# Optimization experiments

Hardware: AMD Instinct MI355X
Metric: run time of the kernel (lower is better)

Reference implementation:

```python
import jax, jax.numpy as jnp
import numpy as np

B, N, DIM = 2, 2048, 256
H, DH, M, NN, FF = 4, 64, 16, 32, 4
POS_DIM = 2 * FF + 1           # 9
EIN = DH                       # edge_input_dim (edge_dim = 0)
STD = 1e-3                     # init_eps


def setup_inputs() -> dict:
    key = jax.random.key(0)
    ks = jax.random.split(key, 16)
    w = lambda k, s: (jax.random.normal(k, s, jnp.float32) * STD)
    z = lambda s: jnp.zeros(s, jnp.float32)
    return {
        'feats': jax.random.normal(ks[0], (B, N, DIM), jnp.float32),
        'coors': jax.random.normal(ks[1], (B, N, 3), jnp.float32),
        'w_qkv': w(ks[2], (DIM, 3 * H * DH)),
        'w_out': w(ks[3], (H * DH, DIM)), 'b_out': z((DIM,)),
        'w_p1': w(ks[4], (POS_DIM, 2 * DH)), 'b_p1': z((2 * DH,)),
        'w_p2': w(ks[5], (2 * DH, DH)), 'b_p2': z((DH,)),
        'w_e1': w(ks[6], (EIN, 2 * EIN)), 'b_e1': z((2 * EIN,)),
        'w_e2': w(ks[7], (2 * EIN, M)), 'b_e2': z((M,)),
        'w_a1': w(ks[8], (M, 4 * M)), 'b_a1': z((4 * M,)),
        'w_a2': w(ks[9], (4 * M, 1)), 'b_a2': z((1,)),
        'w_c1': w(ks[10], (M * H, 4 * M)), 'b_c1': z((4 * M,)),
        'w_c2': w(ks[11], (4 * M, 1)), 'b_c2': z((1,)),
    }


def _forward(feats, coors, w_qkv, w_out, b_out, w_p1, b_p1, w_p2, b_p2,
             w_e1, b_e1, w_e2, b_e2, w_a1, b_a1, w_a2, b_a2,
             w_c1, b_c1, w_c2, b_c2):
    b, n, _ = feats.shape
    # pairwise relative coords / distances, then k-nearest-neighbor selection
    rel = coors[:, :, None, :] - coors[:, None, :, :]            # [b,n,n,3]
    dist = jnp.sqrt(jnp.sum(rel * rel, axis=-1))                 # [b,n,n]
    _, idx = jax.lax.top_k(-dist, NN)                            # smallest NN dists -> [b,n,NN]
    rel_nb = jnp.take_along_axis(rel, idx[..., None], axis=2)    # [b,n,NN,3]
    d_nb = jnp.take_along_axis(dist, idx, axis=2)                # [b,n,NN]
    # fourier encode neighbor distances (gather first -> same math, no [b,h,n,n,9] blowup)
    scales = 2.0 ** jnp.arange(FF, dtype=feats.dtype)
    xs = d_nb[..., None] / scales                                # [b,n,NN,FF]
    fe = jnp.concatenate([jnp.sin(xs), jnp.cos(xs), d_nb[..., None]], axis=-1)  # [b,n,NN,9]
    pos = jax.nn.relu(fe @ w_p1 + b_p1) @ w_p2 + b_p2            # [b,n,NN,DH] (head-invariant)
    # qkv
    q, k, v = jnp.split(feats @ w_qkv, 3, axis=-1)
    heads = lambda t: t.reshape(b, n, H, DH).transpose(0, 2, 1, 3)  # [b,H,n,DH]
    q, k, v = heads(q), heads(k), heads(v)
    idx_h = idx[:, None, :, :, None]                             # [b,1,n,NN,1]
    k_nb = jnp.take_along_axis(k[:, :, None, :, :], idx_h, axis=3)  # [b,H,n,NN,DH]
    v_nb = jnp.take_along_axis(v[:, :, None, :, :], idx_h, axis=3) + pos[:, None]
    # edge message MLP on feature differences + positional embedding
    edge_in = q[:, :, :, None, :] - k_nb + pos[:, None]          # [b,H,n,NN,DH]
    m_ij = jax.nn.relu(jax.nn.relu(edge_in @ w_e1 + b_e1) @ w_e2 + b_e2)  # [b,H,n,NN,M]
    # equivariant coordinate update
    coor_in = m_ij.transpose(0, 2, 3, 1, 4).reshape(b, n, NN, H * M)
    coor_w = (jax.nn.relu(coor_in @ w_c1 + b_c1) @ w_c2 + b_c2)[..., 0]  # [b,n,NN]
    coors_out = jnp.einsum('bij,bijc->bic', coor_w, rel_nb)      # [b,n,3]
    # attention from message MLP
    sim = (jax.nn.relu(m_ij @ w_a1 + b_a1) @ w_a2 + b_a2)[..., 0]  # [b,H,n,NN]
    attn = jax.nn.softmax(sim, axis=-1)
    out = jnp.einsum('bhij,bhijd->bhid', attn, v_nb)             # [b,H,n,DH]
    out = out.transpose(0, 2, 1, 3).reshape(b, n, H * DH) @ w_out + b_out
    return out, coors_out


def reference(feats, coors, w_qkv, w_out, b_out, w_p1, b_p1, w_p2, b_p2,
              w_e1, b_e1, w_e2, b_e2, w_a1, b_a1, w_a2, b_a2,
              w_c1, b_c1, w_c2, b_c2):
    return _forward(feats, coors, w_qkv, w_out, b_out, w_p1, b_p1, w_p2, b_p2,
                    w_e1, b_e1, w_e2, b_e2, w_a1, b_a1, w_a2, b_a2,
                    w_c1, b_c1, w_c2, b_c2)
```

## Files before the change

kernel.cpp:

```cpp
#include <hip/hip_runtime.h>
#include <float.h>
#include <math.h>

#define BB   2
#define NPTS 2048
#define NODES (BB*NPTS)
#define NNB  32
#define NH   4
#define NDH  64

#define SCR_LD  132
#define POS_LD   68
#define M_LD     68
#define E2T_LD  132

__global__ __launch_bounds__(256) void knn_kernel(const float* __restrict__ coors,
    int* __restrict__ idx_out, float* __restrict__ dnb_out, float* __restrict__ rel_out) {
#pragma clang fp contract(off)
  const int node = blockIdx.x;
  const int b = node >> 11;
  const int i = node & (NPTS - 1);
  __shared__ float cx[NPTS], cy[NPTS], cz[NPTS];
  __shared__ float wdist[4]; __shared__ int wjj[4];
  __shared__ float win_d_s; __shared__ int win_j_s;
  __shared__ float sel_d[NNB]; __shared__ int sel_j[NNB];
  const float* cb = coors + (size_t)b * NPTS * 3;
  for (int j = threadIdx.x; j < NPTS; j += 256) {
    cx[j] = cb[3*j]; cy[j] = cb[3*j+1]; cz[j] = cb[3*j+2];
  }
  __syncthreads();
  const float xi = cx[i], yi = cy[i], zi = cz[i];
  float dl[8]; int jl[8];
  #pragma unroll
  for (int s = 0; s < 8; ++s) {
    int j = threadIdx.x + (s << 8);
    float dx = xi - cx[j];
    float dy = yi - cy[j];
    float dz = zi - cz[j];
    float ss = dx*dx + dy*dy;
    ss = ss + dz*dz;
    dl[s] = sqrtf(ss);
    jl[s] = j;
  }
  for (int it = 0; it < NNB; ++it) {
    float bd = FLT_MAX; int bj = 0x7FFFFFFF;
    #pragma unroll
    for (int s = 0; s < 8; ++s)
      if (dl[s] < bd || (dl[s] == bd && jl[s] < bj)) { bd = dl[s]; bj = jl[s]; }
    #pragma unroll
    for (int off = 32; off > 0; off >>= 1) {
      float od = __shfl_down(bd, off, 64);
      int   oj = __shfl_down(bj, off, 64);
      if (od < bd || (od == bd && oj < bj)) { bd = od; bj = oj; }
    }
    if ((threadIdx.x & 63) == 0) { wdist[threadIdx.x >> 6] = bd; wjj[threadIdx.x >> 6] = bj; }
    __syncthreads();
    if (threadIdx.x == 0) {
      float fd = wdist[0]; int fj = wjj[0];
      #pragma unroll
      for (int w = 1; w < 4; ++w)
        if (wdist[w] < fd || (wdist[w] == fd && wjj[w] < fj)) { fd = wdist[w]; fj = wjj[w]; }
      win_d_s = fd; win_j_s = fj; sel_d[it] = fd; sel_j[it] = fj;
    }
    __syncthreads();
    const int wj = win_j_s;
    #pragma unroll
    for (int s = 0; s < 8; ++s) if (jl[s] == wj) dl[s] = FLT_MAX;
    __syncthreads();
  }
  if (threadIdx.x < NNB) {
    int s = threadIdx.x;
    int j = sel_j[s];
    idx_out[(size_t)node*NNB + s] = j;
    dnb_out[(size_t)node*NNB + s] = sel_d[s];
    float* rp = rel_out + ((size_t)node*NNB + s)*3;
    rp[0] = xi - cx[j]; rp[1] = yi - cy[j]; rp[2] = zi - cz[j];
  }
}

template<bool SPLIT>
__global__ __launch_bounds__(256) void gemm_kernel(const float* __restrict__ A,
    const float* __restrict__ Bm, const float* __restrict__ bias,
    float* __restrict__ C0, float* __restrict__ C1, float* __restrict__ C2,
    int Mn, int Nn, int Kn, int lda, int ldb) {
  __shared__ float As[64][17];
  __shared__ __align__(16) float Bs[16][64];
  const int bm = blockIdx.x * 64, bn = blockIdx.y * 64;
  const int tx = threadIdx.x & 15, ty = threadIdx.x >> 4;
  const int lm = threadIdx.x >> 2, lk = (threadIdx.x & 3) * 4;
  const int br = threadIdx.x >> 4, bc = (threadIdx.x & 15) * 4;
  float acc[4][4] = {};
  for (int k0 = 0; k0 < Kn; k0 += 16) {
    float4 av = *(const float4*)(A + (size_t)(bm + lm)*lda + k0 + lk);
    As[lm][lk+0] = av.x; As[lm][lk+1] = av.y; As[lm][lk+2] = av.z; As[lm][lk+3] = av.w;
    float4 bv = *(const float4*)(Bm + (size_t)(k0 + br)*ldb + bn + bc);
    *(float4*)&Bs[br][bc] = bv;
    __syncthreads();
    #pragma unroll
    for (int kk = 0; kk < 16; ++kk) {
      float a0 = As[ty*4+0][kk], a1 = As[ty*4+1][kk], a2 = As[ty*4+2][kk], a3 = As[ty*4+3][kk];
      float4 bq = *(const float4*)&Bs[kk][tx*4];
      acc[0][0] += a0*bq.x; acc[0][1] += a0*bq.y; acc[0][2] += a0*bq.z; acc[0][3] += a0*bq.w;
      acc[1][0] += a1*bq.x; acc[1][1] += a1*bq.y; acc[1][2] += a1*bq.z; acc[1][3] += a1*bq.w;
      acc[2][0] += a2*bq.x; acc[2][1] += a2*bq.y; acc[2][2] += a2*bq.z; acc[2][3] += a2*bq.w;
      acc[3][0] += a3*bq.x; acc[3][1] += a3*bq.y; acc[3][2] += a3*bq.z; acc[3][3] += a3*bq.w;
    }
    __syncthreads();
  }
  #pragma unroll
  for (int r = 0; r < 4; ++r) {
    #pragma unroll
    for (int c = 0; c < 4; ++c) {
      int row = bm + ty*4 + r, col = bn + tx*4 + c;
      float vv = acc[r][c];
      if (bias) vv += bias[col];
      if (SPLIT) {
        int w = col >> 8, cc = col & 255;
        float* Cp = (w == 0) ? C0 : ((w == 1) ? C1 : C2);
        Cp[(size_t)row*256 + cc] = vv;
      } else {
        C0[(size_t)row*Nn + col] = vv;
      }
    }
  }
}

__global__ __launch_bounds__(512, 4) void fused_kernel(
    const int* __restrict__ idx, const float* __restrict__ dnb, const float* __restrict__ relnb,
    const float* __restrict__ qe, const float* __restrict__ ke, const float* __restrict__ v,
    const float* __restrict__ w_p1, const float* __restrict__ b_p1,
    const float* __restrict__ w_p2, const float* __restrict__ b_p2,
    const float* __restrict__ w_e1, const float* __restrict__ w_e2, const float* __restrict__ b_e2,
    const float* __restrict__ w_a1, const float* __restrict__ b_a1,
    const float* __restrict__ w_a2, const float* __restrict__ b_a2,
    const float* __restrict__ w_c1, const float* __restrict__ b_c1,
    const float* __restrict__ w_c2, const float* __restrict__ b_c2,
    float* __restrict__ hsum, float* __restrict__ coors_out) {
  extern __shared__ float sm[];
  float* w_e2Ts= sm;
  float* w_a1s = w_e2Ts + 2112;
  float* qe_s  = w_a1s + 1024;
  float* fe_s  = qe_s + 512;
  float* pos_s = fe_s + 288;
  float* scr   = pos_s + 2176;
  float* m_all = scr + 4224;
  float* sim_s = m_all + 2176;
  float* attn_s= sim_s + 128;
  float* part_s= attn_s + 128;
  float* cw_s  = part_s + 512;
  float* dnb_s = cw_s + 32;
  float* rel_s = dnb_s + 32;
  int*   idx_s = (int*)(rel_s + 96);
  const int t = threadIdx.x;
  const int node = blockIdx.x;
  const int b = node >> 11;

  for (int i = t; i < 2048; i += 512) {
    int kx = i >> 4, mt = i & 15;
    w_e2Ts[mt*E2T_LD + kx] = w_e2[i];
  }
  for (int i = t; i < 1024; i += 512) w_a1s[i] = w_a1[i];
  qe_s[t] = qe[(size_t)node*512 + t];
  if (t < NNB) { idx_s[t] = idx[(size_t)node*NNB + t]; dnb_s[t] = dnb[(size_t)node*NNB + t]; }
  if (t >= 64 && t < 64 + NNB*3) rel_s[t-64] = relnb[(size_t)node*NNB*3 + (t-64)];
  __syncthreads();

  if (t < NNB) {
    float d = dnb_s[t];
    float* f = fe_s + t*9;
    f[0] = sinf(d);          f[1] = sinf(d*0.5f);
    f[2] = sinf(d*0.25f);    f[3] = sinf(d*0.125f);
    f[4] = cosf(d);          f[5] = cosf(d*0.5f);
    f[6] = cosf(d*0.25f);    f[7] = cosf(d*0.125f);
    f[8] = d;
  }
  __syncthreads();

  #pragma unroll
  for (int rep = 0; rep < 8; ++rep) {
    int i2 = t + rep*512;
    int j = i2 >> 7, o = i2 & 127;
    const float* f = fe_s + j*9;
    float acc = b_p1[o];
    #pragma unroll
    for (int r = 0; r < 9; ++r) acc += f[r] * w_p1[r*128 + o];
    scr[j*SCR_LD + o] = fmaxf(acc, 0.0f);
  }
  __syncthreads();

  {
    int j = t >> 4, og = (t & 15) * 4;
    const float* ph = scr + j*SCR_LD;
    float s0=0,s1=0,s2=0,s3=0, u0=0,u1=0,u2=0,u3=0;
    #pragma unroll 8
    for (int kx = 0; kx < 128; kx += 2) {
      float p0 = ph[kx], p1 = ph[kx+1];
      float4 w0 = *(const float4*)(w_p2 + kx*64 + og);
      float4 w1 = *(const float4*)(w_p2 + (kx+1)*64 + og);
      s0 += p0*w0.x; s1 += p0*w0.y; s2 += p0*w0.z; s3 += p0*w0.w;
      u0 += p1*w1.x; u1 += p1*w1.y; u2 += p1*w1.z; u3 += p1*w1.w;
    }
    float4 bp = *(const float4*)(b_p2 + og);
    pos_s[j*POS_LD+og+0] = bp.x + (s0+u0);
    pos_s[j*POS_LD+og+1] = bp.y + (s1+u1);
    pos_s[j*POS_LD+og+2] = bp.z + (s2+u2);
    pos_s[j*POS_LD+og+3] = bp.w + (s3+u3);
  }
  __syncthreads();

  float pr[8];
  #pragma unroll
  for (int rep = 0; rep < 2; ++rep) {
    int i2 = t + rep*512;
    int j = i2 >> 5, og = (i2 & 31) * 4;
    const float* pj = pos_s + j*POS_LD;
    float s0=0,s1=0,s2=0,s3=0, u0=0,u1=0,u2=0,u3=0;
    #pragma unroll 8
    for (int kx = 0; kx < 64; kx += 2) {
      float p0 = pj[kx], p1 = pj[kx+1];
      float4 w0 = *(const float4*)(w_e1 + kx*128 + og);
      float4 w1 = *(const float4*)(w_e1 + (kx+1)*128 + og);
      s0 += p0*w0.x; s1 += p0*w0.y; s2 += p0*w0.z; s3 += p0*w0.w;
      u0 += p1*w1.x; u1 += p1*w1.y; u2 += p1*w1.z; u3 += p1*w1.w;
    }
    pr[rep*4+0] = s0+u0;
    pr[rep*4+1] = s1+u1;
    pr[rep*4+2] = s2+u2;
    pr[rep*4+3] = s3+u3;
  }

  for (int h = 0; h < NH; ++h) {
    #pragma unroll
    for (int rep = 0; rep < 2; ++rep) {
      int i2 = t + rep*512;
      int j = i2 >> 5, og = (i2 & 31) * 4;
      float4 kv = *(const float4*)(ke + ((size_t)(((b << 11) + idx_s[j])*NH + h))*128 + og);
      float4 qv = *(const float4*)(qe_s + h*128 + og);
      float4 hv;
      hv.x = fmaxf(qv.x - kv.x + pr[rep*4+0], 0.0f);
      hv.y = fmaxf(qv.y - kv.y + pr[rep*4+1], 0.0f);
      hv.z = fmaxf(qv.z - kv.z + pr[rep*4+2], 0.0f);
      hv.w = fmaxf(qv.w - kv.w + pr[rep*4+3], 0.0f);
      *(float4*)(scr + j*SCR_LD + og) = hv;
    }
    __syncthreads();
    {
      int j = t >> 4, mt = t & 15;
      const float* hp = scr + j*SCR_LD;
      const float* wt = w_e2Ts + mt*E2T_LD;
      float s0=0,s1=0,s2=0,s3=0;
      #pragma unroll 8
      for (int kx = 0; kx < 128; kx += 4) {
        float4 hv = *(const float4*)(hp + kx);
        float4 wv = *(const float4*)(wt + kx);
        s0 += hv.x*wv.x; s1 += hv.y*wv.y; s2 += hv.z*wv.z; s3 += hv.w*wv.w;
      }
      m_all[j*M_LD + h*16 + mt] = fmaxf(b_e2[mt] + ((s0+s1)+(s2+s3)), 0.0f);
    }
    __syncthreads();
  }

  {
    int j = t >> 4, h = (t >> 2) & 3, qq = t & 3;
    float mreg[16];
    #pragma unroll
    for (int mt = 0; mt < 16; ++mt) mreg[mt] = m_all[j*M_LD + h*16 + mt];
    float acc = 0.0f;
    #pragma unroll
    for (int oi = 0; oi < 16; ++oi) {
      int oo = qq*16 + oi;
      float ah = b_a1[oo];
      #pragma unroll
      for (int mt = 0; mt < 16; ++mt) ah += mreg[mt] * w_a1s[mt*64 + oo];
      acc += fmaxf(ah, 0.0f) * w_a2[oo];
    }
    part_s[t] = acc;
  }
  __syncthreads();
  if (t < 128) {
    int j = t >> 2, h = t & 3;
    const float* pp = part_s + j*16 + h*4;
    sim_s[h*32 + j] = ((pp[0]+pp[1]) + (pp[2]+pp[3])) + b_a2[0];
  }
  __syncthreads();
  if (t < 4) {
    const float* sp = sim_s + t*32;
    float mx = sp[0];
    for (int j = 1; j < 32; ++j) mx = fmaxf(mx, sp[j]);
    float s = 0.0f; float* ap = attn_s + t*32;
    for (int j = 0; j < 32; ++j) { float e = expf(sp[j] - mx); ap[j] = e; s += e; }
    for (int j = 0; j < 32; ++j) ap[j] = ap[j] / s;
  }
  __syncthreads();

  {
    int jh = t >> 8, h = (t >> 6) & 3, dd = t & 63;
    float acc = 0.0f;
    #pragma unroll
    for (int jj = 0; jj < 16; ++jj) {
      int j = jh*16 + jj;
      float vv = v[(size_t)((b << 11) + idx_s[j])*256 + h*64 + dd] + pos_s[j*POS_LD + dd];
      acc += attn_s[h*32 + j] * vv;
    }
    part_s[t] = acc;
  }
  __syncthreads();
  if (t < 256) hsum[(size_t)node*256 + t] = part_s[t] + part_s[t + 256];
  __syncthreads();

  {
    int j = t >> 4, og = (t & 15) * 4;
    const float* mj = m_all + j*M_LD;
    float s0=0,s1=0,s2=0,s3=0, u0=0,u1=0,u2=0,u3=0;
    #pragma unroll 8
    for (int kx = 0; kx < 64; kx += 2) {
      float m0 = mj[kx], m1 = mj[kx+1];
      float4 w0 = *(const float4*)(w_c1 + kx*64 + og);
      float4 w1 = *(const float4*)(w_c1 + (kx+1)*64 + og);
      s0 += m0*w0.x; s1 += m0*w0.y; s2 += m0*w0.z; s3 += m0*w0.w;
      u0 += m1*w1.x; u1 += m1*w1.y; u2 += m1*w1.z; u3 += m1*w1.w;
    }
    float4 bc = *(const float4*)(b_c1 + og);
    scr[j*SCR_LD+og+0] = fmaxf(bc.x + (s0+u0), 0.0f);
    scr[j*SCR_LD+og+1] = fmaxf(bc.y + (s1+u1), 0.0f);
    scr[j*SCR_LD+og+2] = fmaxf(bc.z + (s2+u2), 0.0f);
    scr[j*SCR_LD+og+3] = fmaxf(bc.w + (s3+u3), 0.0f);
  }
  __syncthreads();
  if (t < 128) {
    int j = t >> 2, qq = t & 3;
    const float* cj = scr + j*SCR_LD + qq*16;
    const float* wc = w_c2 + qq*16;
    float acc = 0.0f;
    #pragma unroll
    for (int oo = 0; oo < 16; ++oo) acc += cj[oo] * wc[oo];
    part_s[t] = acc;
  }
  __syncthreads();
  if (t < 32) {
    const float* pp = part_s + t*4;
    cw_s[t] = ((pp[0]+pp[1]) + (pp[2]+pp[3])) + b_c2[0];
  }
  __syncthreads();
  if (t < 3) {
    float acc = 0.0f;
    for (int j = 0; j < 32; ++j) acc += cw_s[j] * rel_s[j*3 + t];
    coors_out[(size_t)node*3 + t] = acc;
  }
}

extern "C" void kernel_launch(void* const* d_in, const int* in_sizes, int n_in,
                              void* d_out, int out_size, void* d_ws, size_t ws_size,
                              hipStream_t stream) {
  const float* feats = (const float*)d_in[0];
  const float* coors = (const float*)d_in[1];
  const float* w_qkv = (const float*)d_in[2];
  const float* w_out = (const float*)d_in[3];
  const float* b_out = (const float*)d_in[4];
  const float* w_p1  = (const float*)d_in[5];
  const float* b_p1  = (const float*)d_in[6];
  const float* w_p2  = (const float*)d_in[7];
  const float* b_p2  = (const float*)d_in[8];
  const float* w_e1  = (const float*)d_in[9];
  const float* b_e1  = (const float*)d_in[10];
  const float* w_e2  = (const float*)d_in[11];
  const float* b_e2  = (const float*)d_in[12];
  const float* w_a1  = (const float*)d_in[13];
  const float* b_a1  = (const float*)d_in[14];
  const float* w_a2  = (const float*)d_in[15];
  const float* b_a2  = (const float*)d_in[16];
  const float* w_c1  = (const float*)d_in[17];
  const float* b_c1  = (const float*)d_in[18];
  const float* w_c2  = (const float*)d_in[19];
  const float* b_c2  = (const float*)d_in[20];

  float* ws   = (float*)d_ws;
  float* q    = ws;
  float* k    = q   + 1048576;
  float* v    = k   + 1048576;
  float* qe   = v   + 1048576;
  float* ke   = qe  + 2097152;
  float* hsum = ke  + 2097152;
  int*   idx  = (int*)(hsum + 1048576);
  float* dnb  = (float*)(idx + 131072);
  float* reln = dnb + 131072;

  float* outF = (float*)d_out;
  float* outC = outF + (size_t)NODES*256;

  knn_kernel<<<dim3(NODES), dim3(256), 0, stream>>>(coors, idx, dnb, reln);

  gemm_kernel<true><<<dim3(64, 12), dim3(256), 0, stream>>>(
      feats, w_qkv, nullptr, q, k, v, 4096, 768, 256, 256, 768);

  gemm_kernel<false><<<dim3(256, 2), dim3(256), 0, stream>>>(
      q, w_e1, b_e1, qe, nullptr, nullptr, 16384, 128, 64, 64, 128);
  gemm_kernel<false><<<dim3(256, 2), dim3(256), 0, stream>>>(
      k, w_e1, nullptr, ke, nullptr, nullptr, 16384, 128, 64, 64, 128);

  constexpr int FUSED_SMEM = 13472 * 4;
  (void)hipFuncSetAttribute(reinterpret_cast<const void*>(fused_kernel),
                            hipFuncAttributeMaxDynamicSharedMemorySize, FUSED_SMEM);
  fused_kernel<<<dim3(NODES), dim3(512), FUSED_SMEM, stream>>>(
      idx, dnb, reln, qe, ke, v,
      w_p1, b_p1, w_p2, b_p2, w_e1, w_e2, b_e2,
      w_a1, b_a1, w_a2, b_a2, w_c1, b_c1, w_c2, b_c2,
      hsum, outC);

  gemm_kernel<false><<<dim3(64, 4), dim3(256), 0, stream>>>(
      hsum, w_out, b_out, outF, nullptr, nullptr, 4096, 256, 256, 256, 256);
}
```

Before: 727.4 us.

## Map each neighbor to one wave so edge MLP stages need no block barriers

Reassigns work so each 64-lane wave owns four neighbors (16 lanes per neighbor) through the positional MLP, edge MLP, attention-logit and coordinate-weight stages. Every shared-memory value is then produced and consumed within the same wave, which removes most __syncthreads calls. Partial-sum reductions go through shuffles instead of shared-memory scratch, and the coordinate MLP moves before the attention-weighted sum. In exchange, each thread does more serial work per stage (longer dot loops, two float4 weight loads), and correctness depends on implicit intra-wave ordering of shared-memory accesses.

After: 684.9 us. 5.8% less time.

```diff
diff --git a/kernel.cpp b/kernel.cpp
--- a/kernel.cpp
+++ b/kernel.cpp
@@ -154,6 +154,10 @@
   const int t = threadIdx.x;
   const int node = blockIdx.x;
   const int b = node >> 11;
+  const int w   = t >> 6;
+  const int l   = t & 63;
+  const int jw  = (w << 2) | (l >> 4);
+  const int l16 = l & 15;
 
   for (int i = t; i < 2048; i += 512) {
     int kx = i >> 4, mt = i & 15;
@@ -165,89 +169,89 @@
   if (t >= 64 && t < 64 + NNB*3) rel_s[t-64] = relnb[(size_t)node*NNB*3 + (t-64)];
   __syncthreads();
 
-  if (t < NNB) {
-    float d = dnb_s[t];
-    float* f = fe_s + t*9;
+  if (l < 4) {
+    int jj = (w << 2) | l;
+    float d = dnb_s[jj];
+    float* f = fe_s + jj*9;
     f[0] = sinf(d);          f[1] = sinf(d*0.5f);
     f[2] = sinf(d*0.25f);    f[3] = sinf(d*0.125f);
     f[4] = cosf(d);          f[5] = cosf(d*0.5f);
     f[6] = cosf(d*0.25f);    f[7] = cosf(d*0.125f);
     f[8] = d;
   }
-  __syncthreads();
-
-  #pragma unroll
-  for (int rep = 0; rep < 8; ++rep) {
-    int i2 = t + rep*512;
-    int j = i2 >> 7, o = i2 & 127;
-    const float* f = fe_s + j*9;
-    float acc = b_p1[o];
-    #pragma unroll
-    for (int r = 0; r < 9; ++r) acc += f[r] * w_p1[r*128 + o];
-    scr[j*SCR_LD + o] = fmaxf(acc, 0.0f);
-  }
-  __syncthreads();
-
-  {
-    int j = t >> 4, og = (t & 15) * 4;
-    const float* ph = scr + j*SCR_LD;
-    float s0=0,s1=0,s2=0,s3=0, u0=0,u1=0,u2=0,u3=0;
+
+  {
+    const int o8 = l16*8;
+    float4 a0 = *(const float4*)(b_p1 + o8);
+    float4 a1 = *(const float4*)(b_p1 + o8 + 4);
+    #pragma unroll
+    for (int r = 0; r < 9; ++r) {
+      float fr = fe_s[jw*9 + r];
+      float4 w0 = *(const float4*)(w_p1 + r*128 + o8);
+      float4 w1 = *(const float4*)(w_p1 + r*128 + o8 + 4);
+      a0.x += fr*w0.x; a0.y += fr*w0.y; a0.z += fr*w0.z; a0.w += fr*w0.w;
+      a1.x += fr*w1.x; a1.y += fr*w1.y; a1.z += fr*w1.z; a1.w += fr*w1.w;
+    }
+    a0.x = fmaxf(a0.x,0.f); a0.y = fmaxf(a0.y,0.f); a0.z = fmaxf(a0.z,0.f); a0.w = fmaxf(a0.w,0.f);
+    a1.x = fmaxf(a1.x,0.f); a1.y = fmaxf(a1.y,0.f); a1.z = fmaxf(a1.z,0.f); a1.w = fmaxf(a1.w,0.f);
+    *(float4*)(scr + jw*SCR_LD + o8)     = a0;
+    *(float4*)(scr + jw*SCR_LD + o8 + 4) = a1;
+  }
+
+  {
+    const int og = l16*4;
+    const float* ph = scr + jw*SCR_LD;
+    float s0=0,s1=0,s2=0,s3=0;
     #pragma unroll 8
-    for (int kx = 0; kx < 128; kx += 2) {
-      float p0 = ph[kx], p1 = ph[kx+1];
-      float4 w0 = *(const float4*)(w_p2 + kx*64 + og);
-      float4 w1 = *(const float4*)(w_p2 + (kx+1)*64 + og);
-      s0 += p0*w0.x; s1 += p0*w0.y; s2 += p0*w0.z; s3 += p0*w0.w;
-      u0 += p1*w1.x; u1 += p1*w1.y; u2 += p1*w1.z; u3 += p1*w1.w;
+    for (int kx = 0; kx < 128; ++kx) {
+      float p = ph[kx];
+      float4 wv = *(const float4*)(w_p2 + kx*64 + og);
+      s0 += p*wv.x; s1 += p*wv.y; s2 += p*wv.z; s3 += p*wv.w;
     }
     float4 bp = *(const float4*)(b_p2 + og);
-    pos_s[j*POS_LD+og+0] = bp.x + (s0+u0);
-    pos_s[j*POS_LD+og+1] = bp.y + (s1+u1);
-    pos_s[j*POS_LD+og+2] = bp.z + (s2+u2);
-    pos_s[j*POS_LD+og+3] = bp.w + (s3+u3);
-  }
-  __syncthreads();
+    pos_s[jw*POS_LD+og+0] = bp.x + s0;
+    pos_s[jw*POS_LD+og+1] = bp.y + s1;
+    pos_s[jw*POS_LD+og+2] = bp.z + s2;
+    pos_s[jw*POS_LD+og+3] = bp.w + s3;
+  }
 
   float pr[8];
-  #pragma unroll
-  for (int rep = 0; rep < 2; ++rep) {
-    int i2 = t + rep*512;
-    int j = i2 >> 5, og = (i2 & 31) * 4;
-    const float* pj = pos_s + j*POS_LD;
-    float s0=0,s1=0,s2=0,s3=0, u0=0,u1=0,u2=0,u3=0;
+  {
+    const int o8 = l16*8;
+    const float* pj = pos_s + jw*POS_LD;
+    float s0=0,s1=0,s2=0,s3=0,s4=0,s5=0,s6=0,s7=0;
     #pragma unroll 8
-    for (int kx = 0; kx < 64; kx += 2) {
-      float p0 = pj[kx], p1 = pj[kx+1];
-      float4 w0 = *(const float4*)(w_e1 + kx*128 + og);
-      float4 w1 = *(const float4*)(w_e1 + (kx+1)*128 + og);
-      s0 += p0*w0.x; s1 += p0*w0.y; s2 += p0*w0.z; s3 += p0*w0.w;
-      u0 += p1*w1.x; u1 += p1*w1.y; u2 += p1*w1.z; u3 += p1*w1.w;
-    }
-    pr[rep*4+0] = s0+u0;
-    pr[rep*4+1] = s1+u1;
-    pr[rep*4+2] = s2+u2;
-    pr[rep*4+3] = s3+u3;
-  }
-
-  for (int h = 0; h < NH; ++h) {
-    #pragma unroll
-    for (int rep = 0; rep < 2; ++rep) {
-      int i2 = t + rep*512;
-      int j = i2 >> 5, og = (i2 & 31) * 4;
-      float4 kv = *(const float4*)(ke + ((size_t)(((b << 11) + idx_s[j])*NH + h))*128 + og);
-      float4 qv = *(const float4*)(qe_s + h*128 + og);
-      float4 hv;
-      hv.x = fmaxf(qv.x - kv.x + pr[rep*4+0], 0.0f);
-      hv.y = fmaxf(qv.y - kv.y + pr[rep*4+1], 0.0f);
-      hv.z = fmaxf(qv.z - kv.z + pr[rep*4+2], 0.0f);
-      hv.w = fmaxf(qv.w - kv.w + pr[rep*4+3], 0.0f);
-      *(float4*)(scr + j*SCR_LD + og) = hv;
-    }
-    __syncthreads();
-    {
-      int j = t >> 4, mt = t & 15;
-      const float* hp = scr + j*SCR_LD;
-      const float* wt = w_e2Ts + mt*E2T_LD;
+    for (int kx = 0; kx < 64; ++kx) {
+      float p = pj[kx];
+      float4 w0 = *(const float4*)(w_e1 + kx*128 + o8);
+      float4 w1 = *(const float4*)(w_e1 + kx*128 + o8 + 4);
+      s0 += p*w0.x; s1 += p*w0.y; s2 += p*w0.z; s3 += p*w0.w;
+      s4 += p*w1.x; s5 += p*w1.y; s6 += p*w1.z; s7 += p*w1.w;
+    }
+    pr[0]=s0; pr[1]=s1; pr[2]=s2; pr[3]=s3; pr[4]=s4; pr[5]=s5; pr[6]=s6; pr[7]=s7;
+  }
+
+  {
+    const size_t kebase = ((size_t)((b << 11) + idx_s[jw])*NH)*128;
+    const int o8 = l16*8;
+    for (int h = 0; h < NH; ++h) {
+      float4 kv0 = *(const float4*)(ke + kebase + h*128 + o8);
+      float4 kv1 = *(const float4*)(ke + kebase + h*128 + o8 + 4);
+      float4 qv0 = *(const float4*)(qe_s + h*128 + o8);
+      float4 qv1 = *(const float4*)(qe_s + h*128 + o8 + 4);
+      float4 h0, h1;
+      h0.x = fmaxf(qv0.x - kv0.x + pr[0], 0.f);
+      h0.y = fmaxf(qv0.y - kv0.y + pr[1], 0.f);
+      h0.z = fmaxf(qv0.z - kv0.z + pr[2], 0.f);
+      h0.w = fmaxf(qv0.w - kv0.w + pr[3], 0.f);
+      h1.x = fmaxf(qv1.x - kv1.x + pr[4], 0.f);
+      h1.y = fmaxf(qv1.y - kv1.y + pr[5], 0.f);
+      h1.z = fmaxf(qv1.z - kv1.z + pr[6], 0.f);
+      h1.w = fmaxf(qv1.w - kv1.w + pr[7], 0.f);
+      *(float4*)(scr + jw*SCR_LD + o8)     = h0;
+      *(float4*)(scr + jw*SCR_LD + o8 + 4) = h1;
+      const float* hp = scr + jw*SCR_LD;
+      const float* wt = w_e2Ts + l16*E2T_LD;
       float s0=0,s1=0,s2=0,s3=0;
       #pragma unroll 8
       for (int kx = 0; kx < 128; kx += 4) {
@@ -255,16 +259,16 @@
         float4 wv = *(const float4*)(wt + kx);
         s0 += hv.x*wv.x; s1 += hv.y*wv.y; s2 += hv.z*wv.z; s3 += hv.w*wv.w;
       }
-      m_all[j*M_LD + h*16 + mt] = fmaxf(b_e2[mt] + ((s0+s1)+(s2+s3)), 0.0f);
-    }
-    __syncthreads();
-  }
-
-  {
-    int j = t >> 4, h = (t >> 2) & 3, qq = t & 3;
+      m_all[jw*M_LD + h*16 + l16] = fmaxf(b_e2[l16] + ((s0+s1)+(s2+s3)), 0.0f);
+    }
+  }
+
+  {
+    const int jj = (w << 2) | (l >> 4);
+    const int hh = (l >> 2) & 3, qq = l & 3;
     float mreg[16];
     #pragma unroll
-    for (int mt = 0; mt < 16; ++mt) mreg[mt] = m_all[j*M_LD + h*16 + mt];
+    for (int mt = 0; mt < 16; ++mt) mreg[mt] = m_all[jj*M_LD + hh*16 + mt];
     float acc = 0.0f;
     #pragma unroll
     for (int oi = 0; oi < 16; ++oi) {
@@ -274,15 +278,40 @@
       for (int mt = 0; mt < 16; ++mt) ah += mreg[mt] * w_a1s[mt*64 + oo];
       acc += fmaxf(ah, 0.0f) * w_a2[oo];
     }
-    part_s[t] = acc;
+    acc += __shfl_down(acc, 2, 4);
+    acc += __shfl_down(acc, 1, 4);
+    if (qq == 0) sim_s[hh*32 + jj] = acc + b_a2[0];
+  }
+
+  {
+    const int og = l16*4;
+    const float* mj = m_all + jw*M_LD;
+    float s0=0,s1=0,s2=0,s3=0;
+    #pragma unroll 8
+    for (int kx = 0; kx < 64; ++kx) {
+      float m0 = mj[kx];
+      float4 wv = *(const float4*)(w_c1 + kx*64 + og);
+      s0 += m0*wv.x; s1 += m0*wv.y; s2 += m0*wv.z; s3 += m0*wv.w;
+    }
+    float4 bc = *(const float4*)(b_c1 + og);
+    float c0 = fmaxf(bc.x + s0, 0.f), c1 = fmaxf(bc.y + s1, 0.f);
+    float c2 = fmaxf(bc.z + s2, 0.f), c3 = fmaxf(bc.w + s3, 0.f);
+    float4 wc = *(const float4*)(w_c2 + og);
+    float part = ((c0*wc.x + c1*wc.y) + (c2*wc.z + c3*wc.w));
+    part += __shfl_down(part, 8, 16);
+    part += __shfl_down(part, 4, 16);
+    part += __shfl_down(part, 2, 16);
+    part += __shfl_down(part, 1, 16);
+    if (l16 == 0) cw_s[jw] = part + b_c2[0];
   }
   __syncthreads();
-  if (t < 128) {
-    int j = t >> 2, h = t & 3;
-    const float* pp = part_s + j*16 + h*4;
-    sim_s[h*32 + j] = ((pp[0]+pp[1]) + (pp[2]+pp[3])) + b_a2[0];
-  }
-  __syncthreads();
+
+  if (t >= 64 && t < 67) {
+    int c = t - 64;
+    float acc = 0.0f;
+    for (int j = 0; j < 32; ++j) acc += cw_s[j] * rel_s[j*3 + c];
+    coors_out[(size_t)node*3 + c] = acc;
+  }
   if (t < 4) {
     const float* sp = sim_s + t*32;
     float mx = sp[0];
@@ -306,47 +335,6 @@
   }
   __syncthreads();
   if (t < 256) hsum[(size_t)node*256 + t] = part_s[t] + part_s[t + 256];
-  __syncthreads();
-
-  {
-    int j = t >> 4, og = (t & 15) * 4;
-    const float* mj = m_all + j*M_LD;
-    float s0=0,s1=0,s2=0,s3=0, u0=0,u1=0,u2=0,u3=0;
-    #pragma unroll 8
-    for (int kx = 0; kx < 64; kx += 2) {
-      float m0 = mj[kx], m1 = mj[kx+1];
-      float4 w0 = *(const float4*)(w_c1 + kx*64 + og);
-      float4 w1 = *(const float4*)(w_c1 + (kx+1)*64 + og);
-      s0 += m0*w0.x; s1 += m0*w0.y; s2 += m0*w0.z; s3 += m0*w0.w;
-      u0 += m1*w1.x; u1 += m1*w1.y; u2 += m1*w1.z; u3 += m1*w1.w;
-    }
-    float4 bc = *(const float4*)(b_c1 + og);
-    scr[j*SCR_LD+og+0] = fmaxf(bc.x + (s0+u0), 0.0f);
-    scr[j*SCR_LD+og+1] = fmaxf(bc.y + (s1+u1), 0.0f);
-    scr[j*SCR_LD+og+2] = fmaxf(bc.z + (s2+u2), 0.0f);
-    scr[j*SCR_LD+og+3] = fmaxf(bc.w + (s3+u3), 0.0f);
-  }
-  __syncthreads();
-  if (t < 128) {
-    int j = t >> 2, qq = t & 3;
-    const float* cj = scr + j*SCR_LD + qq*16;
-    const float* wc = w_c2 + qq*16;
-    float acc = 0.0f;
-    #pragma unroll
-    for (int oo = 0; oo < 16; ++oo) acc += cj[oo] * wc[oo];
-    part_s[t] = acc;
-  }
-  __syncthreads();
-  if (t < 32) {
-    const float* pp = part_s + t*4;
-    cw_s[t] = ((pp[0]+pp[1]) + (pp[2]+pp[3])) + b_c2[0];
-  }
-  __syncthreads();
-  if (t < 3) {
-    float acc = 0.0f;
-    for (int j = 0; j < 32; ++j) acc += cw_s[j] * rel_s[j*3 + t];
-    coors_out[(size_t)node*3 + t] = acc;
-  }
 }
 
 extern "C" void kernel_launch(void* const* d_in, const int* in_sizes, int n_in,
```
